# Performance work log

Hardware: AMD Instinct MI355X
Metric: run time of the kernel (lower is better)

## Reference

```python
import jax, jax.numpy as jnp
import numpy as np

SCALE = 32.0 / 32.0  # alpha / rank
KEEP = 1.0 - 0.05    # dropout keep prob


def setup_inputs() -> dict:
    key = jax.random.key(0)
    kx, kw, ka, kb, km = jax.random.split(key, 5)
    B_, S, D_in, D_out, R = 4, 2048, 4096, 4096, 32
    x = jax.random.normal(kx, (B_, S, D_in), dtype=jnp.float32)
    W = jax.random.normal(kw, (D_out, D_in), dtype=jnp.float32) * (1.0 / np.sqrt(D_in))
    A = jax.random.normal(ka, (D_in, R), dtype=jnp.float32) * (1.0 / np.sqrt(D_in))
    Bm = jax.random.normal(kb, (R, D_out), dtype=jnp.float32) * 0.02
    # deterministic inverted-dropout mask: {0, 1/KEEP}
    drop_mask = (jax.random.uniform(km, (B_, S, D_in)) < KEEP).astype(jnp.float32) / KEEP
    return {"x": x, "W": W, "A": A, "B": Bm, "drop_mask": drop_mask}


def reference(x, W, A, B, drop_mask):
    # base: F.linear(x, W)  -> x @ W.T   [b,s,out]
    base = jnp.einsum("bsi,oi->bso", x, W)
    # lora: dropout(x) @ A @ B, low-rank path (contract rank first)
    lora = jnp.einsum("bsr,ro->bso", jnp.einsum("bsi,ir->bsr", x * drop_mask, A), B)
    return base + SCALE * lora
```

## Files before the change

kernel.cpp:

```cpp
#include <hip/hip_runtime.h>
#include <hip/hip_bf16.h>

typedef short bf16x8 __attribute__((ext_vector_type(8)));
typedef float f32x4  __attribute__((ext_vector_type(4)));

#define DIN  4096
#define DOUT 4096
#define MTOT 8192
#define RNK  32
#define NT   64

union Pk8 { __hip_bfloat16 h[8]; uint4 u; bf16x8 v; };

__device__ __forceinline__ uint4 pack8(float a0,float a1,float a2,float a3,
                                       float b0,float b1,float b2,float b3){
  Pk8 p;
  p.h[0]=__float2bfloat16(a0); p.h[1]=__float2bfloat16(a1);
  p.h[2]=__float2bfloat16(a2); p.h[3]=__float2bfloat16(a3);
  p.h[4]=__float2bfloat16(b0); p.h[5]=__float2bfloat16(b1);
  p.h[6]=__float2bfloat16(b2); p.h[7]=__float2bfloat16(b3);
  return p.u;
}
__device__ __forceinline__ bf16x8 pack8v(float a0,float a1,float a2,float a3,
                                         float b0,float b1,float b2,float b3){
  Pk8 p;
  p.h[0]=__float2bfloat16(a0); p.h[1]=__float2bfloat16(a1);
  p.h[2]=__float2bfloat16(a2); p.h[3]=__float2bfloat16(a3);
  p.h[4]=__float2bfloat16(b0); p.h[5]=__float2bfloat16(b1);
  p.h[6]=__float2bfloat16(b2); p.h[7]=__float2bfloat16(b3);
  return p.v;
}

__device__ __forceinline__ void gload_lds16(const void* g, void* l){
  __builtin_amdgcn_global_load_lds(
      (const __attribute__((address_space(1))) unsigned int*)g,
      (__attribute__((address_space(3))) unsigned int*)l, 16, 0, 0);
}

#define MFMA(A,B,C) __builtin_amdgcn_mfma_f32_16x16x32_bf16(A,B,C,0,0,0)
#define BAR   asm volatile("s_barrier" ::: "memory")
#define SB0   __builtin_amdgcn_sched_barrier(0)
#define PRIO1 __builtin_amdgcn_s_setprio(1)
#define PRIO0 __builtin_amdgcn_s_setprio(0)

__global__ __launch_bounds__(256) void k_conv_w(const float* __restrict__ W,
                                                __hip_bfloat16* __restrict__ Wb){
  size_t i = ((size_t)blockIdx.x*256 + threadIdx.x) * 8;
  float4 a = *(const float4*)(W + i);
  float4 b = *(const float4*)(W + i + 4);
  *(uint4*)(Wb + i) = pack8(a.x,a.y,a.z,a.w,b.x,b.y,b.z,b.w);
}

__global__ __launch_bounds__(256) void k_conv_ab(const float* __restrict__ A,
                                                 const float* __restrict__ B,
                                                 __hip_bfloat16* __restrict__ At,
                                                 __hip_bfloat16* __restrict__ Bt){
  int idx = blockIdx.x*256 + threadIdx.x;
  if (idx < DIN*RNK){
    int k = idx >> 5, r = idx & 31;
    At[(size_t)r*DIN + k] = __float2bfloat16(A[(size_t)k*RNK + r]);
  } else {
    int j = idx - DIN*RNK;
    int n = j >> 5, k = j & 31;
    Bt[(size_t)n*RNK + k] = __float2bfloat16(B[(size_t)k*DOUT + n]);
  }
}

__global__ __launch_bounds__(256) void k_xt(const float* __restrict__ x,
                                            const float* __restrict__ mk,
                                            const __hip_bfloat16* __restrict__ At,
                                            __hip_bfloat16* __restrict__ xb,
                                            __hip_bfloat16* __restrict__ tb){
  __shared__ float sred[4*512];
  const int t = threadIdx.x, w = t >> 6, l = t & 63;
  const int r0 = blockIdx.x * 16;
  const int lane15 = l & 15, kb = l >> 4;
  const size_t rowbase = (size_t)(r0 + lane15) * DIN;
  const int kbase = w * 1024;

  f32x4 acc0 = {0.f,0.f,0.f,0.f}, acc1 = {0.f,0.f,0.f,0.f};
  const __hip_bfloat16* at0 = At + (size_t)lane15*DIN;
  const __hip_bfloat16* at1 = At + (size_t)(16+lane15)*DIN;

  #pragma unroll 2
  for (int kt = 0; kt < 32; ++kt){
    const int k0 = kbase + kt*32 + kb*8;
    float4 xa = *(const float4*)(x  + rowbase + k0);
    float4 xc = *(const float4*)(x  + rowbase + k0 + 4);
    float4 ma = *(const float4*)(mk + rowbase + k0);
    float4 mc = *(const float4*)(mk + rowbase + k0 + 4);
    *(uint4*)(xb + rowbase + k0) = pack8(xa.x,xa.y,xa.z,xa.w,xc.x,xc.y,xc.z,xc.w);
    bf16x8 af = pack8v(xa.x*ma.x,xa.y*ma.y,xa.z*ma.z,xa.w*ma.w,
                       xc.x*mc.x,xc.y*mc.y,xc.z*mc.z,xc.w*mc.w);
    bf16x8 b0 = *(const bf16x8*)(at0 + k0);
    bf16x8 b1 = *(const bf16x8*)(at1 + k0);
    acc0 = MFMA(af, b0, acc0);
    acc1 = MFMA(af, b1, acc1);
  }

  #pragma unroll
  for (int r = 0; r < 4; ++r){
    sred[(w*64+l)*8 + r]     = acc0[r];
    sred[(w*64+l)*8 + 4 + r] = acc1[r];
  }
  __syncthreads();
  #pragma unroll
  for (int e2 = 0; e2 < 2; ++e2){
    int e  = t*2 + e2;
    int el = e >> 3, er = e & 7;
    float s = sred[el*8+er] + sred[512+el*8+er] + sred[1024+el*8+er] + sred[1536+el*8+er];
    int col  = (er>>2)*16 + (el & 15);
    int orow = (el>>4)*4 + (er & 3);
    tb[(size_t)(r0 + orow)*RNK + col] = __float2bfloat16(s);
  }
}

__global__ __launch_bounds__(512) void k_main7(const __hip_bfloat16* __restrict__ xb,
                                               const __hip_bfloat16* __restrict__ Wb,
                                               const __hip_bfloat16* __restrict__ tb,
                                               const __hip_bfloat16* __restrict__ Bt,
                                               float* __restrict__ out){
  __shared__ __align__(16) __hip_bfloat16 lds[65536];
  const int tid = threadIdx.x;
  const int l  = tid & 63, w = tid >> 6;
  const int wm = w >> 2,  wn = w & 3;
  const int lr = l & 15,  kb = l >> 4;
  const int ch = (kb ^ ((l >> 1) & 3)) & 3;
  const int laneA = (wm*128 + lr)*32 + ch*8;
  const int laneB = (wn*64  + lr)*32 + ch*8;
  const int g_row = tid >> 2;
  const int g_ch  = (((tid & 3) ^ ((tid >> 3) & 3))) * 8;

  const int bid  = blockIdx.x;
  const int xcd  = bid & 7;
  const int idx  = bid >> 3;
  const int bm0  = (((xcd >> 1) << 3) + (idx & 7)) * 256;
  const int bn0  = (((xcd & 1) << 3) + (idx >> 3)) * 256;

  f32x4 acc[8][4];

  {
    const __hip_bfloat16* tp = tb + (size_t)(bm0 + wm*128 + lr)*RNK + kb*8;
    const __hip_bfloat16* bp = Bt + (size_t)(bn0 + wn*64  + lr)*RNK + kb*8;
    bf16x8 tf[8], bf[4];
    #pragma unroll
    for (int m = 0; m < 8; ++m) tf[m] = *(const bf16x8*)(tp + m*16*RNK);
    #pragma unroll
    for (int n = 0; n < 4; ++n) bf[n] = *(const bf16x8*)(bp + n*16*RNK);
    const f32x4 z = {0.f,0.f,0.f,0.f};
    #pragma unroll
    for (int m = 0; m < 8; ++m)
      #pragma unroll
      for (int n = 0; n < 4; ++n)
        acc[m][n] = MFMA(tf[m], bf[n], z);
  }
  asm volatile("" ::: "memory");

  auto STAGE = [&](int bb, int ab, int kh, int kt){
    const __hip_bfloat16* g = ab ? Wb : xb;
    const int base0 = ab ? bn0 : bm0;
    const int segb  = bb*32768 + ab*16384 + kh*8192;
    #pragma unroll
    for (int i = 0; i < 2; ++i){
      const __hip_bfloat16* src = g + (size_t)(base0 + i*128 + g_row)*DIN
                                    + kt*64 + kh*32 + g_ch;
      gload_lds16(src, (void*)&lds[segb + i*4096 + w*512]);
    }
  };

  #define ASEG(bb,kh) ((bb)*32768 + (kh)*8192)
  #define BSEG(bb,kh) ((bb)*32768 + 16384 + (kh)*8192)
  #define LDV(off) (*(const bf16x8*)&lds[(off)])

  STAGE(0,0,0,0); STAGE(0,1,0,0); STAGE(0,0,1,0); STAGE(0,1,1,0);
  STAGE(1,0,0,1); STAGE(1,1,0,1);
  STAGE(1,0,1,1); STAGE(1,1,1,1);
  asm volatile("s_waitcnt vmcnt(8)" ::: "memory");
  BAR; SB0;

  bf16x8 aF[8], aS[8], bF[4], bS[4];
  #pragma unroll
  for (int m = 0; m < 8; ++m) aF[m] = LDV(ASEG(0,0) + laneA + m*512);
  #pragma unroll
  for (int n = 0; n < 4; ++n) bF[n] = LDV(BSEG(0,0) + laneB + n*512);

  for (int t = 0; t < NT; ++t){
    const int b = t & 1, bo = b ^ 1;

    BAR; SB0;
    #pragma unroll
    for (int m = 0; m < 8; ++m) aS[m] = LDV(ASEG(b,1) + laneA + m*512);
    #pragma unroll
    for (int n = 0; n < 4; ++n) bS[n] = LDV(BSEG(b,1) + laneB + n*512);
    if (t+2 < NT){ STAGE(b,0,0,t+2); STAGE(b,1,0,t+2); }
    PRIO1;
    #pragma unroll
    for (int m = 0; m < 8; ++m)
      #pragma unroll
      for (int n = 0; n < 4; ++n)
        acc[m][n] = MFMA(aF[m], bF[n], acc[m][n]);
    PRIO0;
    if (t < NT-2)       asm volatile("s_waitcnt vmcnt(8)" ::: "memory");
    else if (t == NT-2) asm volatile("s_waitcnt vmcnt(4)" ::: "memory");

    BAR; SB0;
    if (t+1 < NT){
      #pragma unroll
      for (int m = 0; m < 8; ++m) aF[m] = LDV(ASEG(bo,0) + laneA + m*512);
      #pragma unroll
      for (int n = 0; n < 4; ++n) bF[n] = LDV(BSEG(bo,0) + laneB + n*512);
    }
    if (t+2 < NT){ STAGE(b,0,1,t+2); STAGE(b,1,1,t+2); }
    PRIO1;
    #pragma unroll
    for (int m = 0; m < 8; ++m)
      #pragma unroll
      for (int n = 0; n < 4; ++n)
        acc[m][n] = MFMA(aS[m], bS[n], acc[m][n]);
    PRIO0;
    if (t < NT-2)       asm volatile("s_waitcnt vmcnt(8)" ::: "memory");
    else if (t == NT-2) asm volatile("s_waitcnt vmcnt(0)" ::: "memory");
  }

  const int orow = bm0 + wm*128 + (l>>4)*4;
  const int ocol = bn0 + wn*64  + (l&15);
  #pragma unroll
  for (int m = 0; m < 8; ++m)
    #pragma unroll
    for (int n = 0; n < 4; ++n)
      #pragma unroll
      for (int r = 0; r < 4; ++r)
        out[(size_t)(orow + m*16 + r)*DOUT + ocol + n*16] = acc[m][n][r];
  #undef LDV
  #undef ASEG
  #undef BSEG
}

__global__ void fb_t(const float* __restrict__ x, const float* __restrict__ mk,
                     const float* __restrict__ A, float* __restrict__ tf){
  const int m = blockIdx.x, t = threadIdx.x;
  float acc[RNK];
  #pragma unroll
  for (int r = 0; r < RNK; ++r) acc[r] = 0.f;
  for (int k = t; k < DIN; k += 256){
    float xm = x[(size_t)m*DIN + k] * mk[(size_t)m*DIN + k];
    #pragma unroll
    for (int r = 0; r < RNK; ++r) acc[r] += xm * A[(size_t)k*RNK + r];
  }
  #pragma unroll
  for (int r = 0; r < RNK; ++r){
    float v = acc[r];
    for (int o = 32; o; o >>= 1) v += __shfl_down(v, o);
    if ((t & 63) == 0) atomicAdd(&tf[(size_t)m*RNK + r], v);
  }
}

__global__ void fb_out(const float* __restrict__ x, const float* __restrict__ W,
                       const float* __restrict__ B, const float* __restrict__ tf,
                       float* __restrict__ out){
  size_t idx = (size_t)blockIdx.x*256 + threadIdx.x;
  int m = (int)(idx >> 12), n = (int)(idx & 4095);
  float acc = 0.f;
  for (int k = 0; k < DIN; ++k)
    acc += x[(size_t)m*DIN + k] * W[(size_t)n*DIN + k];
  #pragma unroll
  for (int r = 0; r < RNK; ++r)
    acc += tf[(size_t)m*RNK + r] * B[(size_t)r*DOUT + n];
  out[idx] = acc;
}

extern "C" void kernel_launch(void* const* d_in, const int* in_sizes, int n_in,
                              void* d_out, int out_size, void* d_ws, size_t ws_size,
                              hipStream_t stream) {
  const float* x  = (const float*)d_in[0];
  const float* W  = (const float*)d_in[1];
  const float* A  = (const float*)d_in[2];
  const float* B  = (const float*)d_in[3];
  const float* mk = (const float*)d_in[4];
  float* out = (float*)d_out;

  const size_t OFF_XB = 0;
  const size_t OFF_WB = OFF_XB + (size_t)MTOT*DIN*2;
  const size_t OFF_TB = OFF_WB + (size_t)DOUT*DIN*2;
  const size_t OFF_AT = OFF_TB + (size_t)MTOT*RNK*2;
  const size_t OFF_BT = OFF_AT + (size_t)RNK*DIN*2;
  const size_t NEED   = OFF_BT + (size_t)DIN*RNK*2;

  if (ws_size >= NEED){
    char* ws = (char*)d_ws;
    __hip_bfloat16* xb = (__hip_bfloat16*)(ws + OFF_XB);
    __hip_bfloat16* Wb = (__hip_bfloat16*)(ws + OFF_WB);
    __hip_bfloat16* tb = (__hip_bfloat16*)(ws + OFF_TB);
    __hip_bfloat16* At = (__hip_bfloat16*)(ws + OFF_AT);
    __hip_bfloat16* Bt = (__hip_bfloat16*)(ws + OFF_BT);

    k_conv_w <<<(DOUT*(size_t)DIN)/(256*8), 256, 0, stream>>>(W, Wb);
    k_conv_ab<<<(2*DIN*RNK)/256,            256, 0, stream>>>(A, B, At, Bt);
    k_xt     <<<MTOT/16,                    256, 0, stream>>>(x, mk, At, xb, tb);
    k_main7  <<<(MTOT/256)*(DOUT/256),      512, 0, stream>>>(xb, Wb, tb, Bt, out);
  } else {
    float* tf = (float*)d_ws;
    hipMemsetAsync(tf, 0, (size_t)MTOT*RNK*4, stream);
    fb_t  <<<MTOT, 256, 0, stream>>>(x, mk, A, tf);
    fb_out<<<((size_t)MTOT*DOUT)/256, 256, 0, stream>>>(x, W, B, tf, out);
  }
}
```

Baseline: 358.7 us.

## Restructure main GEMM loop into four half-tile phases with finer LDS prefetch

Replaces the two-phase double-buffered MFMA loop with four phases per k-tile. Each phase loads half of the A fragments (4 instead of 8) and reuses the B fragments across two phases, which roughly halves the register footprint for operand fragments. Global-to-LDS staging is redistributed, and the x-tile's second K-half is now staged one tile ahead rather than two. The intent is to overlap LDS reads with MFMA at a finer grain and relieve register pressure, at the cost of more barriers per iteration and a shallower prefetch for part of the data.

Result: no change. 362.3 us (+1.0%).

```diff
diff --git a/kernel.cpp b/kernel.cpp
--- a/kernel.cpp
+++ b/kernel.cpp
@@ -42,6 +42,7 @@
 #define SB0   __builtin_amdgcn_sched_barrier(0)
 #define PRIO1 __builtin_amdgcn_s_setprio(1)
 #define PRIO0 __builtin_amdgcn_s_setprio(0)
+#define LGK0  asm volatile("s_waitcnt lgkmcnt(0)" ::: "memory")
 
 __global__ __launch_bounds__(256) void k_conv_w(const float* __restrict__ W,
                                                 __hip_bfloat16* __restrict__ Wb){
@@ -115,7 +116,7 @@
   }
 }
 
-__global__ __launch_bounds__(512) void k_main7(const __hip_bfloat16* __restrict__ xb,
+__global__ __launch_bounds__(512) void k_main8(const __hip_bfloat16* __restrict__ xb,
                                                const __hip_bfloat16* __restrict__ Wb,
                                                const __hip_bfloat16* __restrict__ tb,
                                                const __hip_bfloat16* __restrict__ Bt,
@@ -173,53 +174,73 @@
   #define LDV(off) (*(const bf16x8*)&lds[(off)])
 
   STAGE(0,0,0,0); STAGE(0,1,0,0); STAGE(0,0,1,0); STAGE(0,1,1,0);
-  STAGE(1,0,0,1); STAGE(1,1,0,1);
-  STAGE(1,0,1,1); STAGE(1,1,1,1);
-  asm volatile("s_waitcnt vmcnt(8)" ::: "memory");
-  BAR; SB0;
-
-  bf16x8 aF[8], aS[8], bF[4], bS[4];
-  #pragma unroll
-  for (int m = 0; m < 8; ++m) aF[m] = LDV(ASEG(0,0) + laneA + m*512);
-  #pragma unroll
-  for (int n = 0; n < 4; ++n) bF[n] = LDV(BSEG(0,0) + laneB + n*512);
+  STAGE(1,0,0,1); STAGE(1,1,0,1); STAGE(1,1,1,1);
+  asm volatile("s_waitcnt vmcnt(6)" ::: "memory");
+  BAR;
+
+  bf16x8 aE[4], aO[4], bk[4];
 
   for (int t = 0; t < NT; ++t){
-    const int b = t & 1, bo = b ^ 1;
-
-    BAR; SB0;
-    #pragma unroll
-    for (int m = 0; m < 8; ++m) aS[m] = LDV(ASEG(b,1) + laneA + m*512);
-    #pragma unroll
-    for (int n = 0; n < 4; ++n) bS[n] = LDV(BSEG(b,1) + laneB + n*512);
-    if (t+2 < NT){ STAGE(b,0,0,t+2); STAGE(b,1,0,t+2); }
+    const int b = t & 1, bn = b ^ 1;
+
+    #pragma unroll
+    for (int m = 0; m < 4; ++m) aE[m] = LDV(ASEG(b,0) + laneA + m*512);
+    #pragma unroll
+    for (int n = 0; n < 4; ++n) bk[n] = LDV(BSEG(b,0) + laneB + n*512);
+    if (t+1 < NT) STAGE(bn, 0, 1, t+1);
+    asm volatile("s_waitcnt lgkmcnt(4)" ::: "memory");
+    BAR; LGK0; SB0;
     PRIO1;
     #pragma unroll
-    for (int m = 0; m < 8; ++m)
-      #pragma unroll
-      for (int n = 0; n < 4; ++n)
-        acc[m][n] = MFMA(aF[m], bF[n], acc[m][n]);
-    PRIO0;
-    if (t < NT-2)       asm volatile("s_waitcnt vmcnt(8)" ::: "memory");
-    else if (t == NT-2) asm volatile("s_waitcnt vmcnt(4)" ::: "memory");
-
-    BAR; SB0;
-    if (t+1 < NT){
-      #pragma unroll
-      for (int m = 0; m < 8; ++m) aF[m] = LDV(ASEG(bo,0) + laneA + m*512);
-      #pragma unroll
-      for (int n = 0; n < 4; ++n) bF[n] = LDV(BSEG(bo,0) + laneB + n*512);
-    }
-    if (t+2 < NT){ STAGE(b,0,1,t+2); STAGE(b,1,1,t+2); }
+    for (int m = 0; m < 4; ++m)
+      #pragma unroll
+      for (int n = 0; n < 4; ++n)
+        acc[m][n] = MFMA(aE[m], bk[n], acc[m][n]);
+    PRIO0; SB0;
+    BAR;
+
+    #pragma unroll
+    for (int m = 0; m < 4; ++m) aO[m] = LDV(ASEG(b,0) + laneA + (4+m)*512);
+    BAR; LGK0; SB0;
     PRIO1;
     #pragma unroll
-    for (int m = 0; m < 8; ++m)
-      #pragma unroll
-      for (int n = 0; n < 4; ++n)
-        acc[m][n] = MFMA(aS[m], bS[n], acc[m][n]);
-    PRIO0;
-    if (t < NT-2)       asm volatile("s_waitcnt vmcnt(8)" ::: "memory");
+    for (int m = 0; m < 4; ++m)
+      #pragma unroll
+      for (int n = 0; n < 4; ++n)
+        acc[4+m][n] = MFMA(aO[m], bk[n], acc[4+m][n]);
+    PRIO0; SB0;
+    BAR;
+
+    #pragma unroll
+    for (int m = 0; m < 4; ++m) aE[m] = LDV(ASEG(b,1) + laneA + m*512);
+    #pragma unroll
+    for (int n = 0; n < 4; ++n) bk[n] = LDV(BSEG(b,1) + laneB + n*512);
+    if (t+2 < NT){ STAGE(b, 0, 0, t+2); STAGE(b, 1, 0, t+2); }
+    asm volatile("s_waitcnt lgkmcnt(4)" ::: "memory");
+    BAR; LGK0; SB0;
+    PRIO1;
+    #pragma unroll
+    for (int m = 0; m < 4; ++m)
+      #pragma unroll
+      for (int n = 0; n < 4; ++n)
+        acc[m][n] = MFMA(aE[m], bk[n], acc[m][n]);
+    PRIO0; SB0;
+    BAR;
+
+    #pragma unroll
+    for (int m = 0; m < 4; ++m) aO[m] = LDV(ASEG(b,1) + laneA + (4+m)*512);
+    if (t+2 < NT) STAGE(b, 1, 1, t+2);
+    BAR; LGK0; SB0;
+    PRIO1;
+    #pragma unroll
+    for (int m = 0; m < 4; ++m)
+      #pragma unroll
+      for (int n = 0; n < 4; ++n)
+        acc[4+m][n] = MFMA(aO[m], bk[n], acc[4+m][n]);
+    PRIO0; SB0;
+    if (t < NT-2)       asm volatile("s_waitcnt vmcnt(6)" ::: "memory");
     else if (t == NT-2) asm volatile("s_waitcnt vmcnt(0)" ::: "memory");
+    BAR;
   }
 
   const int orow = bm0 + wm*128 + (l>>4)*4;
@@ -297,7 +318,7 @@
     k_conv_w <<<(DOUT*(size_t)DIN)/(256*8), 256, 0, stream>>>(W, Wb);
     k_conv_ab<<<(2*DIN*RNK)/256,            256, 0, stream>>>(A, B, At, Bt);
     k_xt     <<<MTOT/16,                    256, 0, stream>>>(x, mk, At, xb, tb);
-    k_main7  <<<(MTOT/256)*(DOUT/256),      512, 0, stream>>>(xb, Wb, tb, Bt, out);
+    k_main8  <<<(MTOT/256)*(DOUT/256),      512, 0, stream>>>(xb, Wb, tb, Bt, out);
   } else {
     float* tf = (float*)d_ws;
     hipMemsetAsync(tf, 0, (size_t)MTOT*RNK*4, stream);
```
